# Kernel tuning notes

Measured on AMD Instinct MI355X. Metric: run time of the kernel, lower is better.

## Reference

```python
import jax, jax.numpy as jnp
import numpy as np

FILTER_SIZE = 9
WIN_NUMEL = FILTER_SIZE ** 3  # 729
EPS = 1e-06


def _conv3d_valid(x, w):
    # x: [N,1,D,H,W], w: [1,1,k,k,k]; valid padding, stride 1 (matches F.conv3d padding=0)
    return jax.lax.conv_general_dilated(
        x, w, window_strides=(1, 1, 1), padding='VALID',
        dimension_numbers=('NCDHW', 'OIDHW', 'NCDHW'))


def setup_inputs() -> dict:
    key = jax.random.key(0)
    k1, k2 = jax.random.split(key)
    shape = (1, 1, 160, 160, 160)
    I = jax.random.uniform(k1, shape, dtype=jnp.float32)
    J = jax.random.uniform(k2, shape, dtype=jnp.float32)
    filt = jnp.ones((1, 1, FILTER_SIZE, FILTER_SIZE, FILTER_SIZE), dtype=jnp.float32)
    return {'I': I, 'J': J, 'filt': filt}


def reference(I, J, filt):
    I_sum = _conv3d_valid(I, filt)
    J_sum = _conv3d_valid(J, filt)
    I2_sum = _conv3d_valid(I * I, filt)
    J2_sum = _conv3d_valid(J * J, filt)
    IJ_sum = _conv3d_valid(I * J, filt)

    I_mean = I_sum / WIN_NUMEL
    J_mean = J_sum / WIN_NUMEL

    cross = IJ_sum - I_mean * J_sum - J_mean * I_sum + I_mean * J_mean * WIN_NUMEL
    I_var = I2_sum - 2.0 * I_mean * I_sum + (I_mean ** 2) * WIN_NUMEL
    J_var = J2_sum - 2.0 * J_mean * J_sum + (J_mean ** 2) * WIN_NUMEL

    cc = (cross ** 2) / (I_var * J_var + EPS)
    return 1.0 - jnp.mean(cc)
```

## Files before the change

### kernel.cpp

```cpp
#include <hip/hip_runtime.h>

#define NN 160
#define MM 152
#define TO 16
#define TI 24
#define PSTR 28
#define PCH  (TI*PSTR+4)
#define XROW 28
#define XCH  (TO*XROW+4)
#define YROW 20
#define YCH  (TO*YROW+4)
#define ZC 19
#define PL (ZC+8)
#define KMAX (PL+2)
#define NZ 8
#define NTX 10
#define NTILE 100
#define NBLK (NTILE*NZ)
#define INV_WIN (1.0f/729.0f)

__device__ __forceinline__ float cc_of(const float* s) {
    float cross = fmaf(-s[0] * s[1], INV_WIN, s[4]);
    float iv    = fmaf(-s[0] * s[0], INV_WIN, s[2]);
    float jv    = fmaf(-s[1] * s[1], INV_WIN, s[3]);
    return (cross * cross) / (iv * jv + 1e-6f);
}

__global__ __launch_bounds__(256, 4) void lncc_fused(
    const float* __restrict__ I, const float* __restrict__ J,
    float* __restrict__ partial)
{
    __shared__ float Pld[2 * PCH];
    __shared__ float xsb[2][5 * XCH];
    __shared__ float ysb[2][5 * YCH];
    __shared__ float red[4];

    const int tid  = threadIdx.x;
    const int orig = blockIdx.x;
    const int bid  = (orig & 7) * NTILE + (orig >> 3);
    const int tile = bid % NTILE;
    const int zc   = bid / NTILE;
    const int x0 = (tile % NTX) * TO;
    const int y0 = (tile / NTX) * TO;
    const int z0 = zc * ZC;

    const int yl = tid >> 4, xl = tid & 15;
    const bool valid = (x0 + xl < MM) && (y0 + yl < MM);

    const int lrow = tid / 6;
    const int lq   = tid - 6 * lrow;
    const int gy   = min(y0 + lrow, NN - 1);
    const int gx   = min(x0 + lq * 4, NN - 4);
    const size_t pbase = (size_t)gy * NN + gx;

    const int rowX = tid >> 2;
    const int xbX  = (tid & 3) * 4;

    const int eY = tid - 96;
    const int cY = eY >> 4;
    const int xY = eY & 15;

    float4 pI, pJ;
    if (tid < 144) {
        size_t a = (size_t)z0 * (NN * NN) + pbase;
        pI = *(const float4*)(I + a);
        pJ = *(const float4*)(J + a);
    }

    float ring[9][5];
    float sz[5] = {0.f, 0.f, 0.f, 0.f, 0.f};
    float cc_acc = 0.f;

    for (int kb = 0; kb <= KMAX; kb += 9) {
#pragma unroll
        for (int ki = 0; ki < 9; ++ki) {
            const int k = kb + ki;
            if (k > KMAX) continue;

            if (k >= 1 && k <= PL && tid < 96) {
                const int b = (k - 1) & 1;
                const float4* Ir = (const float4*)&Pld[rowX * PSTR + xbX];
                const float4* Jr = (const float4*)&Pld[PCH + rowX * PSTR + xbX];
                float4 i0 = Ir[0], i1 = Ir[1], i2 = Ir[2];
                float4 j0 = Jr[0], j1 = Jr[1], j2 = Jr[2];
                float iv[12], jv[12];
                iv[0]=i0.x; iv[1]=i0.y; iv[2]=i0.z; iv[3]=i0.w;
                iv[4]=i1.x; iv[5]=i1.y; iv[6]=i1.z; iv[7]=i1.w;
                iv[8]=i2.x; iv[9]=i2.y; iv[10]=i2.z; iv[11]=i2.w;
                jv[0]=j0.x; jv[1]=j0.y; jv[2]=j0.z; jv[3]=j0.w;
                jv[4]=j1.x; jv[5]=j1.y; jv[6]=j1.z; jv[7]=j1.w;
                jv[8]=j2.x; jv[9]=j2.y; jv[10]=j2.z; jv[11]=j2.w;
#pragma unroll
                for (int c = 0; c < 5; ++c) {
                    float m[12];
#pragma unroll
                    for (int t = 0; t < 12; ++t) {
                        float av = (c & 1) ? jv[t] : iv[t];
                        float bv = (c < 2) ? 1.0f : ((c == 2) ? iv[t] : jv[t]);
                        m[t] = av * bv;
                    }
                    float s = m[0]+m[1]+m[2]+m[3]+m[4]+m[5]+m[6]+m[7]+m[8];
                    float* W = &xsb[b][c * XCH + rowX];
                    W[xbX * XROW] = s;
#pragma unroll
                    for (int t = 1; t < 4; ++t) {
                        s += m[t + 8] - m[t - 1];
                        W[(xbX + t) * XROW] = s;
                    }
                }
            }
            if (k >= 2 && k <= PL + 1 && tid >= 96 && tid < 176) {
                const int b = (k - 2) & 1;
                const float4* R = (const float4*)&xsb[b][cY * XCH + xY * XROW];
                float4 w0 = R[0], w1 = R[1], w2 = R[2], w3 = R[3], w4 = R[4], w5 = R[5];
                float m[24];
                m[0]=w0.x;  m[1]=w0.y;  m[2]=w0.z;  m[3]=w0.w;
                m[4]=w1.x;  m[5]=w1.y;  m[6]=w1.z;  m[7]=w1.w;
                m[8]=w2.x;  m[9]=w2.y;  m[10]=w2.z; m[11]=w2.w;
                m[12]=w3.x; m[13]=w3.y; m[14]=w3.z; m[15]=w3.w;
                m[16]=w4.x; m[17]=w4.y; m[18]=w4.z; m[19]=w4.w;
                m[20]=w5.x; m[21]=w5.y; m[22]=w5.z; m[23]=w5.w;
                float o[16];
                float s = m[0]+m[1]+m[2]+m[3]+m[4]+m[5]+m[6]+m[7]+m[8];
                o[0] = s;
#pragma unroll
                for (int t = 1; t < 16; ++t) {
                    s += m[t + 8] - m[t - 1];
                    o[t] = s;
                }
                float4* Wv = (float4*)&ysb[b][cY * YCH + xY * YROW];
                float4 oa = {o[0],  o[1],  o[2],  o[3]};
                float4 ob = {o[4],  o[5],  o[6],  o[7]};
                float4 oc = {o[8],  o[9],  o[10], o[11]};
                float4 od = {o[12], o[13], o[14], o[15]};
                Wv[0] = oa; Wv[1] = ob; Wv[2] = oc; Wv[3] = od;
            }
            __syncthreads();

            if (k <= PL - 1 && tid < 144) {
                *(float4*)&Pld[lrow * PSTR + lq * 4]       = pI;
                *(float4*)&Pld[PCH + lrow * PSTR + lq * 4] = pJ;
                if (k <= PL - 2) {
                    size_t adr = (size_t)(z0 + k + 1) * (NN * NN) + pbase;
                    pI = *(const float4*)(I + adr);
                    pJ = *(const float4*)(J + adr);
                }
            }
            if (k >= 3) {
                const int b = (k - 3) & 1;
                const int slot  = (ki + 6) % 9;
                const int slot2 = (ki + 7) % 9;
                float v[5];
#pragma unroll
                for (int c = 0; c < 5; ++c) {
                    v[c] = ysb[b][c * YCH + xl * YROW + yl];
                    sz[c] += v[c];
                    ring[slot][c] = v[c];
                }
                if (k >= 11) {
                    cc_acc += valid ? cc_of(sz) : 0.f;
#pragma unroll
                    for (int c = 0; c < 5; ++c) sz[c] -= ring[slot2][c];
                }
            }
            __syncthreads();
        }
    }

    for (int off = 32; off > 0; off >>= 1)
        cc_acc += __shfl_down(cc_acc, off, 64);
    if ((tid & 63) == 0) red[tid >> 6] = cc_acc;
    __syncthreads();
    if (tid == 0) partial[orig] = red[0] + red[1] + red[2] + red[3];
}

__global__ __launch_bounds__(256) void lncc_final(
    const float* __restrict__ partial, float* __restrict__ out)
{
    double s = 0.0;
    for (int i = threadIdx.x; i < NBLK; i += 256)
        s += (double)partial[i];
    for (int off = 32; off > 0; off >>= 1)
        s += __shfl_down(s, off, 64);
    __shared__ double red[4];
    const int lane = threadIdx.x & 63, wid = threadIdx.x >> 6;
    if (lane == 0) red[wid] = s;
    __syncthreads();
    if (threadIdx.x == 0) {
        double tot = red[0] + red[1] + red[2] + red[3];
        out[0] = (float)(1.0 - tot / ((double)MM * MM * MM));
    }
}

extern "C" void kernel_launch(void* const* d_in, const int* in_sizes, int n_in,
                              void* d_out, int out_size, void* d_ws, size_t ws_size,
                              hipStream_t stream) {
    const float* I = (const float*)d_in[0];
    const float* J = (const float*)d_in[1];

    float* partial = (float*)d_ws;

    lncc_fused<<<NBLK, 256, 0, stream>>>(I, J, partial);
    lncc_final<<<1,    256, 0, stream>>>(partial, (float*)d_out);
    (void)in_sizes; (void)n_in; (void)out_size; (void)ws_size;
}
```

Baseline: 41.26 us.

## Store x-pass results row-major and vectorize y-pass with float4 column sums

The x-pass now writes its four sliding sums as one float4 into a row-major shared buffer instead of transposed scalar stores. The y-pass is reassigned to 40 threads in the fourth wavefront, each summing a 4-wide by 8-row patch with float4 loads and adds. The z-pass read becomes row-major as well. This is meant to cut scalar LDS stores and bank conflicts and to move y-pass work onto an otherwise idle wave, at the cost of fewer y-pass threads each doing more work.

```diff
diff --git a/kernel.cpp b/kernel.cpp
--- a/kernel.cpp
+++ b/kernel.cpp
@@ -6,10 +6,10 @@
 #define TI 24
 #define PSTR 28
 #define PCH  (TI*PSTR+4)
-#define XROW 28
-#define XCH  (TO*XROW+4)
-#define YROW 20
-#define YCH  (TO*YROW+4)
+#define XR   20
+#define XCH  (TI*XR+4)
+#define YR   20
+#define YCH  (TO*YR+4)
 #define ZC 19
 #define PL (ZC+8)
 #define KMAX (PL+2)
@@ -26,6 +26,13 @@
     return (cross * cross) / (iv * jv + 1e-6f);
 }
 
+__device__ __forceinline__ float4 f4add(float4 a, float4 b) {
+    float4 r; r.x=a.x+b.x; r.y=a.y+b.y; r.z=a.z+b.z; r.w=a.w+b.w; return r;
+}
+__device__ __forceinline__ float4 f4sub(float4 a, float4 b) {
+    float4 r; r.x=a.x-b.x; r.y=a.y-b.y; r.z=a.z-b.z; r.w=a.w-b.w; return r;
+}
+
 __global__ __launch_bounds__(256, 4) void lncc_fused(
     const float* __restrict__ I, const float* __restrict__ J,
     float* __restrict__ partial)
@@ -56,9 +63,10 @@
     const int rowX = tid >> 2;
     const int xbX  = (tid & 3) * 4;
 
-    const int eY = tid - 96;
-    const int cY = eY >> 4;
-    const int xY = eY & 15;
+    const int eY  = tid - 192;
+    const int cY  = eY >> 3;
+    const int xbY = ((eY >> 1) & 3) * 4;
+    const int ybY = (eY & 1) * 8;
 
     float4 pI, pJ;
     if (tid < 144) {
@@ -99,41 +107,30 @@
                         float bv = (c < 2) ? 1.0f : ((c == 2) ? iv[t] : jv[t]);
                         m[t] = av * bv;
                     }
-                    float s = m[0]+m[1]+m[2]+m[3]+m[4]+m[5]+m[6]+m[7]+m[8];
-                    float* W = &xsb[b][c * XCH + rowX];
-                    W[xbX * XROW] = s;
-#pragma unroll
-                    for (int t = 1; t < 4; ++t) {
-                        s += m[t + 8] - m[t - 1];
-                        W[(xbX + t) * XROW] = s;
-                    }
-                }
-            }
-            if (k >= 2 && k <= PL + 1 && tid >= 96 && tid < 176) {
+                    float s0 = m[0]+m[1]+m[2]+m[3]+m[4]+m[5]+m[6]+m[7]+m[8];
+                    float s1 = s0 + m[9]  - m[0];
+                    float s2 = s1 + m[10] - m[1];
+                    float s3 = s2 + m[11] - m[2];
+                    float4 o; o.x = s0; o.y = s1; o.z = s2; o.w = s3;
+                    *(float4*)&xsb[b][c * XCH + rowX * XR + xbX] = o;
+                }
+            }
+            if (k >= 2 && k <= PL + 1 && tid >= 192 && tid < 232) {
                 const int b = (k - 2) & 1;
-                const float4* R = (const float4*)&xsb[b][cY * XCH + xY * XROW];
-                float4 w0 = R[0], w1 = R[1], w2 = R[2], w3 = R[3], w4 = R[4], w5 = R[5];
-                float m[24];
-                m[0]=w0.x;  m[1]=w0.y;  m[2]=w0.z;  m[3]=w0.w;
-                m[4]=w1.x;  m[5]=w1.y;  m[6]=w1.z;  m[7]=w1.w;
-                m[8]=w2.x;  m[9]=w2.y;  m[10]=w2.z; m[11]=w2.w;
-                m[12]=w3.x; m[13]=w3.y; m[14]=w3.z; m[15]=w3.w;
-                m[16]=w4.x; m[17]=w4.y; m[18]=w4.z; m[19]=w4.w;
-                m[20]=w5.x; m[21]=w5.y; m[22]=w5.z; m[23]=w5.w;
-                float o[16];
-                float s = m[0]+m[1]+m[2]+m[3]+m[4]+m[5]+m[6]+m[7]+m[8];
-                o[0] = s;
-#pragma unroll
-                for (int t = 1; t < 16; ++t) {
-                    s += m[t + 8] - m[t - 1];
-                    o[t] = s;
-                }
-                float4* Wv = (float4*)&ysb[b][cY * YCH + xY * YROW];
-                float4 oa = {o[0],  o[1],  o[2],  o[3]};
-                float4 ob = {o[4],  o[5],  o[6],  o[7]};
-                float4 oc = {o[8],  o[9],  o[10], o[11]};
-                float4 od = {o[12], o[13], o[14], o[15]};
-                Wv[0] = oa; Wv[1] = ob; Wv[2] = oc; Wv[3] = od;
+                const float* Rb = &xsb[b][cY * XCH + xbY];
+                float4 w[16];
+#pragma unroll
+                for (int j = 0; j < 16; ++j)
+                    w[j] = *(const float4*)&Rb[(ybY + j) * XR];
+                float4 o = f4add(f4add(f4add(f4add(w[0], w[1]), f4add(w[2], w[3])),
+                                 f4add(f4add(w[4], w[5]), f4add(w[6], w[7]))), w[8]);
+                float* Wb = &ysb[b][cY * YCH + xbY];
+                *(float4*)&Wb[ybY * YR] = o;
+#pragma unroll
+                for (int t = 1; t < 8; ++t) {
+                    o = f4add(o, f4sub(w[t + 8], w[t - 1]));
+                    *(float4*)&Wb[(ybY + t) * YR] = o;
+                }
             }
             __syncthreads();
 
@@ -153,7 +150,7 @@
                 float v[5];
 #pragma unroll
                 for (int c = 0; c < 5; ++c) {
-                    v[c] = ysb[b][c * YCH + xl * YROW + yl];
+                    v[c] = ysb[b][c * YCH + yl * YR + xl];
                     sz[c] += v[c];
                     ring[slot][c] = v[c];
                 }
```

Measured after the change: 51.70 us. 1.25x slower.
